# Kernel optimization log

Hardware: AMD Instinct MI355X
Metric: run time of the kernel (lower is better)

## Reference

```python
import jax, jax.numpy as jnp
import numpy as np

R = 16            # full voxel grid resolution -> N = R**3 = 4096 tokens
WS = 8            # window size -> (R//WS)**3 = 8 windows of WS**3 = 512 tokens
C = 1024          # channels
H = 16            # num heads
D = C // H        # head dim = 64
FREQ_DIM = D // 2 // 3   # rope freqs per spatial axis = 10
HALF = D // 2            # 32 complex pairs per head
ROPE_LO, ROPE_HI = 1.0, 10000.0


def setup_inputs() -> dict:
    key = jax.random.key(0)
    k0, k1, k2 = jax.random.split(key, 3)
    g = jnp.arange(R, dtype=jnp.int32)
    zz, yy, xx = jnp.meshgrid(g, g, g, indexing='ij')
    N = R ** 3
    coords = jnp.stack([jnp.zeros(N, jnp.int32), zz.ravel(), yy.ravel(), xx.ravel()], axis=-1)  # [N,4]
    x = jax.random.normal(k0, (N, C), jnp.float32)
    w_qkv = jax.random.normal(k1, (C, 3 * C), jnp.float32) * np.float32(C ** -0.5)
    b_qkv = jnp.zeros((3 * C,), jnp.float32)
    w_out = jax.random.normal(k2, (C, C), jnp.float32) * np.float32(C ** -0.5)
    b_out = jnp.zeros((C,), jnp.float32)
    q_gamma = jnp.ones((H, D), jnp.float32)
    k_gamma = jnp.ones((H, D), jnp.float32)
    return dict(x=x, coords=coords, w_qkv=w_qkv, b_qkv=b_qkv,
                q_gamma=q_gamma, k_gamma=k_gamma, w_out=w_out, b_out=b_out)


def _mh_rms_norm(t, gamma):
    # SparseMultiHeadRMSNorm: F.normalize(x, dim=-1) * gamma * sqrt(D), computed in fp32
    t = t.astype(jnp.float32)
    n = jnp.linalg.norm(t, axis=-1, keepdims=True)
    return t / jnp.maximum(n, 1e-12) * gamma * np.float32(np.sqrt(D))


def _forward(x, coords, w_qkv, b_qkv, q_gamma, k_gamma, w_out, b_out):
    N = x.shape[0]
    qkv = (x @ w_qkv + b_qkv).reshape(N, 3, H, D)
    q, k, v = qkv[:, 0], qkv[:, 1], qkv[:, 2]
    # qk rms norm
    q = _mh_rms_norm(q, q_gamma)
    k = _mh_rms_norm(k, k_gamma)
    # RoPE: phases from 3D coords, freq_dim per axis, zero-phase padding to HALF
    freqs = ROPE_LO / (ROPE_HI ** (jnp.arange(FREQ_DIM, dtype=jnp.float32) / FREQ_DIM))
    ang = (coords[:, 1:].astype(jnp.float32)[..., None] * freqs).reshape(N, 3 * FREQ_DIM)
    ang = jnp.pad(ang, ((0, 0), (0, HALF - 3 * FREQ_DIM)))   # padded phases = 0 (identity rotation)
    cosp = jnp.cos(ang)[:, None, :]   # [N,1,HALF]
    sinp = jnp.sin(ang)[:, None, :]

    def rope(t):
        tr = t.reshape(N, H, HALF, 2)
        re, im = tr[..., 0], tr[..., 1]
        return jnp.stack([re * cosp - im * sinp, re * sinp + im * cosp], -1).reshape(N, H, D)

    q, k = rope(q), rope(k)
    # window partition (calc_window_partition): full grid -> all windows have WS**3 tokens
    nw = R // WS
    wc = coords[:, 1:] // WS
    widx = (wc[:, 0] * nw + wc[:, 1]) * nw + wc[:, 2]   # batch coord is 0
    order = jnp.argsort(widx)        # fwd_indices
    inv = jnp.argsort(order)         # bwd_indices
    L = WS ** 3
    W = N // L
    qw = q[order].reshape(W, L, H, D)
    kw = k[order].reshape(W, L, H, D)
    vw = v[order].reshape(W, L, H, D)
    att = jnp.einsum('wlhd,wmhd->whlm', qw, kw) * np.float32(1.0 / np.sqrt(D))
    att = jax.nn.softmax(att, axis=-1)
    o = jnp.einsum('whlm,wmhd->wlhd', att, vw).reshape(N, C)
    o = o[inv]                        # scatter back to original token order
    return o @ w_out + b_out


def reference(x, coords, w_qkv, b_qkv, q_gamma, k_gamma, w_out, b_out):
    return _forward(x, coords, w_qkv, b_qkv, q_gamma, k_gamma, w_out, b_out)
```

## Files before the change

### kernel.cpp

```cpp
#include <hip/hip_runtime.h>
#include <math.h>

namespace {

typedef _Float16 f16_t;
typedef __attribute__((ext_vector_type(8))) _Float16 f16x8;
typedef __attribute__((ext_vector_type(4))) float f32x4;

constexpr int kN = 4096;
constexpr int kC = 1024;
constexpr int kH = 16;
constexpr int kD = 64;
constexpr int kL = 512;

__device__ __forceinline__ void gload16(const void* g, void* l) {
  __builtin_amdgcn_global_load_lds(
      (const __attribute__((address_space(1))) unsigned int*)g,
      (__attribute__((address_space(3))) unsigned int*)l, 16, 0, 0);
}

__global__ __launch_bounds__(256) void pack_rows_f16(
    const float* __restrict__ src, f16_t* __restrict__ dst, int M, int K) {
  __shared__ __align__(16) f16_t Th[64][72];
  const int t = threadIdx.x;
  const int m0 = blockIdx.x * 64, k0 = blockIdx.y * 64;
#pragma unroll
  for (int it = 0; it < 4; ++it) {
    const int slot = it * 256 + t;
    const int m = slot >> 4;
    const int k4 = (slot & 15) * 4;
    const float4 v = *(const float4*)&src[(size_t)(m0 + m) * K + k0 + k4];
    Th[m][k4 + 0] = (f16_t)v.x;
    Th[m][k4 + 1] = (f16_t)v.y;
    Th[m][k4 + 2] = (f16_t)v.z;
    Th[m][k4 + 3] = (f16_t)v.w;
  }
  __syncthreads();
#pragma unroll
  for (int it = 0; it < 2; ++it) {
    const int slot = it * 256 + t;
    const int kcl = slot >> 6;
    const int m = slot & 63;
    const size_t o = ((size_t)(blockIdx.y * 8 + kcl) * M + m0 + m) * 8;
    *(f16x8*)&dst[o] = *(const f16x8*)&Th[m][kcl * 8];
  }
}

__global__ __launch_bounds__(256) void pack_w_f16(
    const float* __restrict__ src, f16_t* __restrict__ dst, int K, int N) {
  const int n = blockIdx.x * 256 + threadIdx.x;
  const int kcg = blockIdx.y;
  f16x8 h;
#pragma unroll
  for (int j = 0; j < 8; ++j)
    h[j] = (f16_t)src[(size_t)(kcg * 8 + j) * N + n];
  *(f16x8*)&dst[((size_t)kcg * N + n) * 8] = h;
}

__global__ __launch_bounds__(256) void gemm_f16(
    const f16_t* __restrict__ A, const f16_t* __restrict__ B,
    const float* __restrict__ bias, float* __restrict__ C, int M, int N,
    int K) {
  __shared__ __align__(16) f16_t As[4][128][8];
  __shared__ __align__(16) f16_t Bs[4][128][8];

  const int t = threadIdx.x;
  const int lane = t & 63;
  const int wid = t >> 6;
  const int wr = wid >> 1, wc = wid & 1;
  const int l15 = lane & 15, lk = lane >> 4;
  const int row0 = blockIdx.y * 128, col0 = blockIdx.x * 128;

  f32x4 acc[4][4];
#pragma unroll
  for (int i = 0; i < 4; ++i)
#pragma unroll
    for (int j = 0; j < 4; ++j) acc[i][j] = (f32x4){0.f, 0.f, 0.f, 0.f};

  for (int k0 = 0; k0 < K; k0 += 32) {
    const int kq = k0 >> 3;
#pragma unroll
    for (int s = 0; s < 2; ++s) {
      const int li = s * 256 + t;
      const int kc = li >> 7;
      const int r = li & 127;
      const size_t goff = (size_t)(kq + kc);
      char* adst = (char*)(&As[0][0][0]) + (size_t)(s * 256 + wid * 64) * 16;
      char* bdst = (char*)(&Bs[0][0][0]) + (size_t)(s * 256 + wid * 64) * 16;
      gload16(&A[(goff * M + row0 + r) * 8], adst);
      gload16(&B[(goff * N + col0 + r) * 8], bdst);
    }
    __syncthreads();

    f16x8 af[4], bf[4];
#pragma unroll
    for (int f = 0; f < 4; ++f) {
      af[f] = *(const f16x8*)&As[lk][wr * 64 + f * 16 + l15][0];
      bf[f] = *(const f16x8*)&Bs[lk][wc * 64 + f * 16 + l15][0];
    }
#pragma unroll
    for (int mf = 0; mf < 4; ++mf)
#pragma unroll
      for (int nf = 0; nf < 4; ++nf)
        acc[mf][nf] = __builtin_amdgcn_mfma_f32_16x16x32_f16(
            af[mf], bf[nf], acc[mf][nf], 0, 0, 0);
    __syncthreads();
  }

#pragma unroll
  for (int mf = 0; mf < 4; ++mf)
#pragma unroll
    for (int nf = 0; nf < 4; ++nf) {
      const int col = col0 + wc * 64 + nf * 16 + l15;
      const float bv = bias[col];
#pragma unroll
      for (int r = 0; r < 4; ++r) {
        const int row = row0 + wr * 64 + mf * 16 + lk * 4 + r;
        C[(size_t)row * N + col] = acc[mf][nf][r] + bv;
      }
    }
}

__global__ __launch_bounds__(256) void post_qkv(
    const float* __restrict__ qkv, const int* __restrict__ coords,
    const float* __restrict__ qg, const float* __restrict__ kg,
    f16_t* __restrict__ qwF, f16_t* __restrict__ kwF,
    f16_t* __restrict__ vwF) {
  const int token = blockIdx.x * 4 + (threadIdx.x >> 6);
  const int t = threadIdx.x & 63;
  const int h = t >> 2;
  const int quad = t & 3;
  const int d0 = quad * 16;

  const float* base = qkv + (size_t)token * (3 * kC) + h * kD + d0;
  float qv[16], kv[16], vv[16];
#pragma unroll
  for (int i = 0; i < 16; i += 4) {
    *(float4*)&qv[i] = *(const float4*)&base[i];
    *(float4*)&kv[i] = *(const float4*)&base[kC + i];
    *(float4*)&vv[i] = *(const float4*)&base[2 * kC + i];
  }

  float sq = 0.f, sk = 0.f;
#pragma unroll
  for (int i = 0; i < 16; ++i) {
    sq += qv[i] * qv[i];
    sk += kv[i] * kv[i];
  }
  sq += __shfl_xor(sq, 1);
  sq += __shfl_xor(sq, 2);
  sk += __shfl_xor(sk, 1);
  sk += __shfl_xor(sk, 2);
  const float qs = 8.0f / fmaxf(sqrtf(sq), 1e-12f);
  const float ks = 8.0f / fmaxf(sqrtf(sk), 1e-12f);

#pragma unroll
  for (int i = 0; i < 16; ++i) {
    qv[i] *= qs * qg[h * kD + d0 + i];
    kv[i] *= ks * kg[h * kD + d0 + i];
  }

  const int cz = coords[token * 4 + 1];
  const int cy = coords[token * 4 + 2];
  const int cx = coords[token * 4 + 3];

#pragma unroll
  for (int jj = 0; jj < 8; ++jj) {
    const int j = quad * 8 + jj;
    float ang = 0.f;
    if (j < 30) {
      const int axis = j / 10;
      const int f = j - axis * 10;
      const float coord = (float)(axis == 0 ? cz : (axis == 1 ? cy : cx));
      const float freq = expf(-(float)f * 0.92103403719761836f);
      ang = coord * freq;
    }
    float sn, cs;
    sincosf(ang, &sn, &cs);
    const float qre = qv[2 * jj], qim = qv[2 * jj + 1];
    qv[2 * jj + 0] = qre * cs - qim * sn;
    qv[2 * jj + 1] = qre * sn + qim * cs;
    const float kre = kv[2 * jj], kim = kv[2 * jj + 1];
    kv[2 * jj + 0] = kre * cs - kim * sn;
    kv[2 * jj + 1] = kre * sn + kim * cs;
  }

  const int w = ((cz >> 3) * 2 + (cy >> 3)) * 2 + (cx >> 3);
  const int p = ((cz & 7) * 8 + (cy & 7)) * 8 + (cx & 7);
  const int whq = w * kH + h;
  f16_t* qo = qwF + (size_t)whq * 32768;
  f16_t* ko = kwF + (size_t)whq * 32768;
  f16_t* vo = vwF + (size_t)whq * 32768;

  f16x8 qh[2], kh[2];
#pragma unroll
  for (int c = 0; c < 2; ++c)
#pragma unroll
    for (int j = 0; j < 8; ++j) {
      qh[c][j] = (f16_t)(qv[c * 8 + j] * 0.125f);
      kh[c][j] = (f16_t)kv[c * 8 + j];
    }
  const int kq0 = quad * 2;
  *(f16x8*)&qo[((kq0 + 0) * kL + p) * 8] = qh[0];
  *(f16x8*)&qo[((kq0 + 1) * kL + p) * 8] = qh[1];
  *(f16x8*)&ko[((kq0 + 0) * kL + p) * 8] = kh[0];
  *(f16x8*)&ko[((kq0 + 1) * kL + p) * 8] = kh[1];

  const int ck = p >> 3, jv = p & 7;
#pragma unroll
  for (int i = 0; i < 16; ++i)
    vo[(ck * 64 + d0 + i) * 8 + jv] = (f16_t)vv[i];
}

__global__ __launch_bounds__(256) void attn_mfma(
    const f16_t* __restrict__ qw, const f16_t* __restrict__ kw,
    const f16_t* __restrict__ vw, f16_t* __restrict__ ob) {
  __shared__ __align__(16) f16_t Ks[8 * 64 * 8];
  __shared__ __align__(16) f16_t Vs[8 * 64 * 8];
  __shared__ __align__(16) f16_t Ps[4][32][72];

  const int bid = blockIdx.x;
  const int qt = bid & 3;
  const int h = (bid >> 2) & 15;
  const int w = bid >> 6;
  const int t = threadIdx.x;
  const int lane = t & 63;
  const int wid = t >> 6;
  const int l15 = lane & 15, lk = lane >> 4;
  const int whq = w * kH + h;
  const f16_t* qbase = qw + (size_t)whq * 32768;
  const f16_t* kbase = kw + (size_t)whq * 32768;
  const f16_t* vbase = vw + (size_t)whq * 32768;

  const int qrow0 = qt * 128 + wid * 32;

  f16x8 aq[2][2];
#pragma unroll
  for (int m = 0; m < 2; ++m)
#pragma unroll
    for (int ks = 0; ks < 2; ++ks)
      aq[m][ks] = *(const f16x8*)&qbase[((ks * 4 + lk) * kL + qrow0 +
                                         m * 16 + l15) * 8];

  f32x4 oacc[2][4];
  float mrun[2][4], lrun[2][4];
#pragma unroll
  for (int m = 0; m < 2; ++m)
#pragma unroll
    for (int i = 0; i < 4; ++i) {
      mrun[m][i] = -1e30f;
      lrun[m][i] = 0.f;
    }
#pragma unroll
  for (int m = 0; m < 2; ++m)
#pragma unroll
    for (int nf = 0; nf < 4; ++nf) oacc[m][nf] = (f32x4){0.f, 0.f, 0.f, 0.f};

  for (int kt = 0; kt < 8; ++kt) {
    __syncthreads();
#pragma unroll
    for (int s = 0; s < 2; ++s) {
      const int idx = s * 256 + t;
      const int bidx = s * 256 + wid * 64;
      gload16(&kbase[((idx >> 6) * kL + kt * 64 + (idx & 63)) * 8],
              (char*)Ks + (size_t)bidx * 16);
      gload16(&vbase[((kt * 8 + (idx >> 6)) * 64 + (idx & 63)) * 8],
              (char*)Vs + (size_t)bidx * 16);
    }
    __syncthreads();

    f32x4 sacc[2][4];
#pragma unroll
    for (int m = 0; m < 2; ++m)
#pragma unroll
      for (int nf = 0; nf < 4; ++nf) sacc[m][nf] = (f32x4){0.f, 0.f, 0.f, 0.f};
#pragma unroll
    for (int ks = 0; ks < 2; ++ks) {
      f16x8 bk[4];
#pragma unroll
      for (int nf = 0; nf < 4; ++nf)
        bk[nf] = *(const f16x8*)&Ks[((ks * 4 + lk) * 64 + nf * 16 + l15) * 8];
#pragma unroll
      for (int m = 0; m < 2; ++m)
#pragma unroll
        for (int nf = 0; nf < 4; ++nf)
          sacc[m][nf] = __builtin_amdgcn_mfma_f32_16x16x32_f16(
              aq[m][ks], bk[nf], sacc[m][nf], 0, 0, 0);
    }

#pragma unroll
    for (int m = 0; m < 2; ++m)
#pragma unroll
      for (int i = 0; i < 4; ++i) {
        float rmax = fmaxf(fmaxf(sacc[m][0][i], sacc[m][1][i]),
                           fmaxf(sacc[m][2][i], sacc[m][3][i]));
        rmax = fmaxf(rmax, __shfl_xor(rmax, 1));
        rmax = fmaxf(rmax, __shfl_xor(rmax, 2));
        rmax = fmaxf(rmax, __shfl_xor(rmax, 4));
        rmax = fmaxf(rmax, __shfl_xor(rmax, 8));
        const float mn = fmaxf(mrun[m][i], rmax);
        const float corr = __expf(mrun[m][i] - mn);
        mrun[m][i] = mn;
        float p[4];
        float rs = 0.f;
#pragma unroll
        for (int nf = 0; nf < 4; ++nf) {
          p[nf] = __expf(sacc[m][nf][i] - mn);
          rs += p[nf];
        }
        rs += __shfl_xor(rs, 1);
        rs += __shfl_xor(rs, 2);
        rs += __shfl_xor(rs, 4);
        rs += __shfl_xor(rs, 8);
        lrun[m][i] = lrun[m][i] * corr + rs;
#pragma unroll
        for (int nf = 0; nf < 4; ++nf) oacc[m][nf][i] *= corr;
        const int row = m * 16 + lk * 4 + i;
#pragma unroll
        for (int nf = 0; nf < 4; ++nf)
          Ps[wid][row][nf * 16 + l15] = (f16_t)p[nf];
      }

#pragma unroll
    for (int ks = 0; ks < 2; ++ks) {
      f16x8 pa[2], bv[4];
#pragma unroll
      for (int m = 0; m < 2; ++m)
        pa[m] = *(const f16x8*)&Ps[wid][m * 16 + l15][ks * 32 + lk * 8];
#pragma unroll
      for (int nf = 0; nf < 4; ++nf)
        bv[nf] = *(const f16x8*)&Vs[((ks * 4 + lk) * 64 + nf * 16 + l15) * 8];
#pragma unroll
      for (int m = 0; m < 2; ++m)
#pragma unroll
        for (int nf = 0; nf < 4; ++nf)
          oacc[m][nf] = __builtin_amdgcn_mfma_f32_16x16x32_f16(
              pa[m], bv[nf], oacc[m][nf], 0, 0, 0);
    }
  }

  const int wz = w >> 2, wy = (w >> 1) & 1, wx = w & 1;
#pragma unroll
  for (int m = 0; m < 2; ++m)
#pragma unroll
    for (int i = 0; i < 4; ++i) {
      const int pg = qrow0 + m * 16 + lk * 4 + i;
      const int pz = pg >> 6, py = (pg >> 3) & 7, px = pg & 7;
      const int n = ((wz * 8 + pz) * 16 + wy * 8 + py) * 16 + wx * 8 + px;
      const float inv = 1.0f / lrun[m][i];
#pragma unroll
      for (int nf = 0; nf < 4; ++nf) {
        const int c0 = h * kD + nf * 16 + l15;
        ob[((size_t)(c0 >> 3) * kN + n) * 8 + (c0 & 7)] =
            (f16_t)(oacc[m][nf][i] * inv);
      }
    }
}

}

extern "C" void kernel_launch(void* const* d_in, const int* in_sizes, int n_in,
                              void* d_out, int out_size, void* d_ws,
                              size_t ws_size, hipStream_t stream) {
  const float* x = (const float*)d_in[0];
  const int* coords = (const int*)d_in[1];
  const float* w_qkv = (const float*)d_in[2];
  const float* b_qkv = (const float*)d_in[3];
  const float* qg = (const float*)d_in[4];
  const float* kg = (const float*)d_in[5];
  const float* w_out = (const float*)d_in[6];
  const float* b_out = (const float*)d_in[7];
  float* out = (float*)d_out;

  char* ws8 = (char*)d_ws;
  float* qkv = (float*)ws8;
  f16_t* obF = (f16_t*)ws8;
  f16_t* BoF = (f16_t*)(ws8 + 8388608);
  char* r1 = ws8 + 50331648;
  f16_t* AF = (f16_t*)r1;
  f16_t* BqF = (f16_t*)(r1 + 8388608);
  f16_t* qwF = (f16_t*)r1;
  f16_t* kwF = (f16_t*)(r1 + 8388608);
  f16_t* vwF = (f16_t*)(r1 + 16777216);

  pack_rows_f16<<<dim3(kN / 64, kC / 64), 256, 0, stream>>>(x, AF, kN, kC);
  pack_w_f16<<<dim3(3 * kC / 256, kC / 8), 256, 0, stream>>>(w_qkv, BqF, kC,
                                                             3 * kC);
  gemm_f16<<<dim3(3 * kC / 128, kN / 128), 256, 0, stream>>>(
      AF, BqF, b_qkv, qkv, kN, 3 * kC, kC);
  post_qkv<<<dim3(kN / 4), 256, 0, stream>>>(qkv, coords, qg, kg, qwF, kwF,
                                             vwF);
  attn_mfma<<<dim3(4 * kH * 8), 256, 0, stream>>>(qwF, kwF, vwF, obF);
  pack_w_f16<<<dim3(kC / 256, kC / 8), 256, 0, stream>>>(w_out, BoF, kC, kC);
  gemm_f16<<<dim3(kC / 128, kN / 128), 256, 0, stream>>>(
      obF, BoF, b_out, out, kN, kC, kC);
}
```

Before: 220.3 us.

## Fuse QK RMS-norm, RoPE and window scatter into the QKV GEMM epilogue

```diff
diff --git a/kernel.cpp b/kernel.cpp
--- a/kernel.cpp
+++ b/kernel.cpp
@@ -121,95 +121,126 @@
     }
 }
 
-__global__ __launch_bounds__(256) void post_qkv(
-    const float* __restrict__ qkv, const int* __restrict__ coords,
+__global__ __launch_bounds__(256) void gemm_qkv(
+    const f16_t* __restrict__ A, const f16_t* __restrict__ B,
+    const float* __restrict__ bias, const int* __restrict__ coords,
     const float* __restrict__ qg, const float* __restrict__ kg,
     f16_t* __restrict__ qwF, f16_t* __restrict__ kwF,
     f16_t* __restrict__ vwF) {
-  const int token = blockIdx.x * 4 + (threadIdx.x >> 6);
-  const int t = threadIdx.x & 63;
-  const int h = t >> 2;
-  const int quad = t & 3;
-  const int d0 = quad * 16;
-
-  const float* base = qkv + (size_t)token * (3 * kC) + h * kD + d0;
-  float qv[16], kv[16], vv[16];
-#pragma unroll
-  for (int i = 0; i < 16; i += 4) {
-    *(float4*)&qv[i] = *(const float4*)&base[i];
-    *(float4*)&kv[i] = *(const float4*)&base[kC + i];
-    *(float4*)&vv[i] = *(const float4*)&base[2 * kC + i];
-  }
-
-  float sq = 0.f, sk = 0.f;
-#pragma unroll
-  for (int i = 0; i < 16; ++i) {
-    sq += qv[i] * qv[i];
-    sk += kv[i] * kv[i];
-  }
-  sq += __shfl_xor(sq, 1);
-  sq += __shfl_xor(sq, 2);
-  sk += __shfl_xor(sk, 1);
-  sk += __shfl_xor(sk, 2);
-  const float qs = 8.0f / fmaxf(sqrtf(sq), 1e-12f);
-  const float ks = 8.0f / fmaxf(sqrtf(sk), 1e-12f);
-
-#pragma unroll
-  for (int i = 0; i < 16; ++i) {
-    qv[i] *= qs * qg[h * kD + d0 + i];
-    kv[i] *= ks * kg[h * kD + d0 + i];
-  }
-
-  const int cz = coords[token * 4 + 1];
-  const int cy = coords[token * 4 + 2];
-  const int cx = coords[token * 4 + 3];
-
-#pragma unroll
-  for (int jj = 0; jj < 8; ++jj) {
-    const int j = quad * 8 + jj;
-    float ang = 0.f;
-    if (j < 30) {
-      const int axis = j / 10;
-      const int f = j - axis * 10;
-      const float coord = (float)(axis == 0 ? cz : (axis == 1 ? cy : cx));
-      const float freq = expf(-(float)f * 0.92103403719761836f);
-      ang = coord * freq;
-    }
-    float sn, cs;
-    sincosf(ang, &sn, &cs);
-    const float qre = qv[2 * jj], qim = qv[2 * jj + 1];
-    qv[2 * jj + 0] = qre * cs - qim * sn;
-    qv[2 * jj + 1] = qre * sn + qim * cs;
-    const float kre = kv[2 * jj], kim = kv[2 * jj + 1];
-    kv[2 * jj + 0] = kre * cs - kim * sn;
-    kv[2 * jj + 1] = kre * sn + kim * cs;
-  }
-
-  const int w = ((cz >> 3) * 2 + (cy >> 3)) * 2 + (cx >> 3);
-  const int p = ((cz & 7) * 8 + (cy & 7)) * 8 + (cx & 7);
-  const int whq = w * kH + h;
-  f16_t* qo = qwF + (size_t)whq * 32768;
-  f16_t* ko = kwF + (size_t)whq * 32768;
-  f16_t* vo = vwF + (size_t)whq * 32768;
-
-  f16x8 qh[2], kh[2];
-#pragma unroll
-  for (int c = 0; c < 2; ++c)
-#pragma unroll
-    for (int j = 0; j < 8; ++j) {
-      qh[c][j] = (f16_t)(qv[c * 8 + j] * 0.125f);
-      kh[c][j] = (f16_t)kv[c * 8 + j];
-    }
-  const int kq0 = quad * 2;
-  *(f16x8*)&qo[((kq0 + 0) * kL + p) * 8] = qh[0];
-  *(f16x8*)&qo[((kq0 + 1) * kL + p) * 8] = qh[1];
-  *(f16x8*)&ko[((kq0 + 0) * kL + p) * 8] = kh[0];
-  *(f16x8*)&ko[((kq0 + 1) * kL + p) * 8] = kh[1];
-
-  const int ck = p >> 3, jv = p & 7;
-#pragma unroll
-  for (int i = 0; i < 16; ++i)
-    vo[(ck * 64 + d0 + i) * 8 + jv] = (f16_t)vv[i];
+  constexpr int M = kN, N = 3 * kC, K = kC;
+  __shared__ __align__(16) f16_t As[4][128][8];
+  __shared__ __align__(16) f16_t Bs[4][128][8];
+
+  const int t = threadIdx.x;
+  const int lane = t & 63;
+  const int wid = t >> 6;
+  const int wr = wid >> 1, wc = wid & 1;
+  const int l15 = lane & 15, lk = lane >> 4;
+  const int row0 = blockIdx.y * 128, col0 = blockIdx.x * 128;
+
+  f32x4 acc[4][4];
+#pragma unroll
+  for (int i = 0; i < 4; ++i)
+#pragma unroll
+    for (int j = 0; j < 4; ++j) acc[i][j] = (f32x4){0.f, 0.f, 0.f, 0.f};
+
+  for (int k0 = 0; k0 < K; k0 += 32) {
+    const int kq = k0 >> 3;
+#pragma unroll
+    for (int s = 0; s < 2; ++s) {
+      const int li = s * 256 + t;
+      const int kc = li >> 7;
+      const int r = li & 127;
+      const size_t goff = (size_t)(kq + kc);
+      char* adst = (char*)(&As[0][0][0]) + (size_t)(s * 256 + wid * 64) * 16;
+      char* bdst = (char*)(&Bs[0][0][0]) + (size_t)(s * 256 + wid * 64) * 16;
+      gload16(&A[(goff * M + row0 + r) * 8], adst);
+      gload16(&B[(goff * N + col0 + r) * 8], bdst);
+    }
+    __syncthreads();
+
+    f16x8 af[4], bf[4];
+#pragma unroll
+    for (int f = 0; f < 4; ++f) {
+      af[f] = *(const f16x8*)&As[lk][wr * 64 + f * 16 + l15][0];
+      bf[f] = *(const f16x8*)&Bs[lk][wc * 64 + f * 16 + l15][0];
+    }
+#pragma unroll
+    for (int mf = 0; mf < 4; ++mf)
+#pragma unroll
+      for (int nf = 0; nf < 4; ++nf)
+        acc[mf][nf] = __builtin_amdgcn_mfma_f32_16x16x32_f16(
+            af[mf], bf[nf], acc[mf][nf], 0, 0, 0);
+    __syncthreads();
+  }
+
+  const int cb = col0 + wc * 64;
+  const int tsel = cb >> 10;
+  const int h = (cb >> 6) & 15;
+  f16_t* obase = (tsel == 0 ? qwF : (tsel == 1 ? kwF : vwF));
+
+  float bv[4], gv[4], freq[4];
+  int axis[4];
+#pragma unroll
+  for (int nf = 0; nf < 4; ++nf) {
+    bv[nf] = bias[cb + nf * 16 + l15];
+    gv[nf] = (tsel == 0) ? qg[h * kD + nf * 16 + l15]
+             : (tsel == 1) ? kg[h * kD + nf * 16 + l15] : 1.f;
+    const int j = nf * 8 + (l15 >> 1);
+    axis[nf] = (j >= 10) + (j >= 20);
+    freq[nf] = (j < 30)
+                   ? expf(-(float)(j - axis[nf] * 10) * 0.92103403719761836f)
+                   : 0.f;
+  }
+  const float sgn = (l15 & 1) ? 1.f : -1.f;
+
+#pragma unroll
+  for (int mf = 0; mf < 4; ++mf)
+#pragma unroll
+    for (int r = 0; r < 4; ++r) {
+      const int row = row0 + wr * 64 + mf * 16 + lk * 4 + r;
+      const int4 cc = *(const int4*)&coords[row * 4];
+      const int w = ((cc.y >> 3) * 2 + (cc.z >> 3)) * 2 + (cc.w >> 3);
+      const int p = ((cc.y & 7) * 8 + (cc.z & 7)) * 8 + (cc.w & 7);
+      f16_t* ob = obase + (size_t)(w * kH + h) * 32768;
+
+      float v[4];
+#pragma unroll
+      for (int nf = 0; nf < 4; ++nf) v[nf] = acc[mf][nf][r] + bv[nf];
+
+      if (tsel < 2) {
+        float s = v[0] * v[0] + v[1] * v[1] + v[2] * v[2] + v[3] * v[3];
+        s += __shfl_xor(s, 1);
+        s += __shfl_xor(s, 2);
+        s += __shfl_xor(s, 4);
+        s += __shfl_xor(s, 8);
+        const float sc = 8.0f / fmaxf(sqrtf(s), 1e-12f);
+#pragma unroll
+        for (int nf = 0; nf < 4; ++nf) v[nf] *= sc * gv[nf];
+#pragma unroll
+        for (int nf = 0; nf < 4; ++nf) {
+          const float c =
+              (float)(axis[nf] == 0 ? cc.y : (axis[nf] == 1 ? cc.z : cc.w));
+          const float ang = c * freq[nf];
+          float sn, cs;
+          __sincosf(ang, &sn, &cs);
+          const float partner = __shfl_xor(v[nf], 1);
+          v[nf] = v[nf] * cs + sgn * sn * partner;
+        }
+        const float qsc = (tsel == 0) ? 0.125f : 1.f;
+#pragma unroll
+        for (int nf = 0; nf < 4; ++nf) {
+          const int d = nf * 16 + l15;
+          ob[((d >> 3) * kL + p) * 8 + (d & 7)] = (f16_t)(v[nf] * qsc);
+        }
+      } else {
+#pragma unroll
+        for (int nf = 0; nf < 4; ++nf) {
+          const int d = nf * 16 + l15;
+          ob[((p >> 3) * kD + d) * 8 + (p & 7)] = (f16_t)v[nf];
+        }
+      }
+    }
 }
 
 __global__ __launch_bounds__(256) void attn_mfma(
@@ -323,19 +354,19 @@
 
 #pragma unroll
     for (int ks = 0; ks < 2; ++ks) {
-      f16x8 pa[2], bv[4];
+      f16x8 pa[2], bvv[4];
 #pragma unroll
       for (int m = 0; m < 2; ++m)
         pa[m] = *(const f16x8*)&Ps[wid][m * 16 + l15][ks * 32 + lk * 8];
 #pragma unroll
       for (int nf = 0; nf < 4; ++nf)
-        bv[nf] = *(const f16x8*)&Vs[((ks * 4 + lk) * 64 + nf * 16 + l15) * 8];
+        bvv[nf] = *(const f16x8*)&Vs[((ks * 4 + lk) * 64 + nf * 16 + l15) * 8];
 #pragma unroll
       for (int m = 0; m < 2; ++m)
 #pragma unroll
         for (int nf = 0; nf < 4; ++nf)
           oacc[m][nf] = __builtin_amdgcn_mfma_f32_16x16x32_f16(
-              pa[m], bv[nf], oacc[m][nf], 0, 0, 0);
+              pa[m], bvv[nf], oacc[m][nf], 0, 0, 0);
     }
   }
 
@@ -373,25 +404,21 @@
   float* out = (float*)d_out;
 
   char* ws8 = (char*)d_ws;
-  float* qkv = (float*)ws8;
-  f16_t* obF = (f16_t*)ws8;
-  f16_t* BoF = (f16_t*)(ws8 + 8388608);
-  char* r1 = ws8 + 50331648;
-  f16_t* AF = (f16_t*)r1;
-  f16_t* BqF = (f16_t*)(r1 + 8388608);
-  f16_t* qwF = (f16_t*)r1;
-  f16_t* kwF = (f16_t*)(r1 + 8388608);
-  f16_t* vwF = (f16_t*)(r1 + 16777216);
+  f16_t* AF = (f16_t*)ws8;
+  f16_t* BqF = (f16_t*)(ws8 + 8388608);
+  f16_t* BoF = (f16_t*)(ws8 + 16777216);
+  f16_t* qwF = (f16_t*)(ws8 + 33554432);
+  f16_t* kwF = (f16_t*)(ws8 + 41943040);
+  f16_t* vwF = (f16_t*)(ws8 + 50331648);
+  f16_t* obF = (f16_t*)(ws8 + 58720256);
 
   pack_rows_f16<<<dim3(kN / 64, kC / 64), 256, 0, stream>>>(x, AF, kN, kC);
   pack_w_f16<<<dim3(3 * kC / 256, kC / 8), 256, 0, stream>>>(w_qkv, BqF, kC,
                                                              3 * kC);
-  gemm_f16<<<dim3(3 * kC / 128, kN / 128), 256, 0, stream>>>(
-      AF, BqF, b_qkv, qkv, kN, 3 * kC, kC);
-  post_qkv<<<dim3(kN / 4), 256, 0, stream>>>(qkv, coords, qg, kg, qwF, kwF,
-                                             vwF);
+  pack_w_f16<<<dim3(kC / 256, kC / 8), 256, 0, stream>>>(w_out, BoF, kC, kC);
+  gemm_qkv<<<dim3(3 * kC / 128, kN / 128), 256, 0, stream>>>(
+      AF, BqF, b_qkv, coords, qg, kg, qwF, kwF, vwF);
   attn_mfma<<<dim3(4 * kH * 8), 256, 0, stream>>>(qwF, kwF, vwF, obF);
-  pack_w_f16<<<dim3(kC / 256, kC / 8), 256, 0, stream>>>(w_out, BoF, kC, kC);
   gemm_f16<<<dim3(kC / 128, kN / 128), 256, 0, stream>>>(
       obF, BoF, b_out, out, kN, kC, kC);
 }
```

Result: faster. 199.6 us (-9.4%).
